# Optimization experiments

Measured on AMD Instinct MI355X. Metric: run time of the kernel, lower is better.

Reference implementation:

```python
import jax, jax.numpy as jnp
import numpy as np

MARGIN = 0.02
EPS = 1e-12


def setup_inputs() -> dict:
    key = jax.random.key(0)
    n, d, k = 4096, 128, 4  # n anchors, embed dim, instances per class
    inputs = jax.random.normal(key, (n, d), dtype=jnp.float32)
    # Balanced, class-grouped batch (required by the original resize trick):
    # label of sample i is i // k.
    targets = (jnp.arange(n) // k).astype(jnp.int32)
    return {"inputs": inputs, "targets": targets, "num_instances": k}


def reference(inputs, targets, num_instances):
    n = inputs.shape[0]
    k = num_instances  # static python int

    # Pairwise euclidean distances (same math as euclidean_dist)
    sq = jnp.sum(inputs * inputs, axis=1, keepdims=True)  # [n,1]
    dist = sq + sq.T - 2.0 * (inputs @ inputs.T)          # [n,n]
    dist = jnp.sqrt(jnp.clip(dist, EPS, None))

    # Structured pos/neg indices for a grouped balanced batch
    # (equivalent to masked_select + resize in the original).
    row = jnp.arange(n)
    class_start = (row // k) * k        # first index of anchor's class block
    pos_in_class = row % k              # anchor's slot within its class
    o_pos = jnp.arange(k - 1)
    # same-class indices excluding self -> [n, k-1]
    pos_idx = class_start[:, None] + o_pos[None, :] + (o_pos[None, :] >= pos_in_class[:, None])
    o_neg = jnp.arange(n - k)
    # all indices outside the anchor's class block -> [n, n-k]
    neg_idx = o_neg[None, :] + k * (o_neg[None, :] >= class_start[:, None])

    pos_dist = dist[row[:, None], pos_idx]  # [n, k-1]
    neg_dist = dist[row[:, None], neg_idx]  # [n, n-k]

    # Triplet margin matrix per anchor: trip[i, m, j] = d_pos[i,j] - d_neg[i,m] + margin
    trip = pos_dist[:, None, :] - neg_dist[:, :, None] + MARGIN  # [n, n-k, k-1]
    mask = trip > 0
    num_valid = jnp.sum(mask)
    total = jnp.sum(jnp.where(mask, trip, 0.0))
    denom = jnp.maximum(num_valid, 1).astype(trip.dtype)
    loss = jnp.where(num_valid > 0, total / denom, jnp.zeros((), trip.dtype))

    per_anchor_valid = jnp.sum(mask, axis=(1, 2))  # [n]
    accuracy = jnp.mean((per_anchor_valid == 0).astype(jnp.float32))
    pos_d = jnp.mean(pos_dist)
    neg_d = jnp.mean(neg_dist)
    return loss, accuracy, pos_d, neg_d
```

## Files before the change

### kernel.cpp

```cpp
#include <hip/hip_runtime.h>

#define NROWS 4096
#define DIM   128
#define KCLS  4
#define NBLK  1056
#define MARGIN_F 0.02f
#define EPS_F    1e-12f

typedef unsigned short ushort_t;
typedef unsigned int   uint_t;
typedef __attribute__((ext_vector_type(8)))  short bf16x8;
typedef __attribute__((ext_vector_type(16))) float f32x16;

__device__ __forceinline__ ushort_t rne_bf16(float v, float& back) {
    uint_t u = __float_as_uint(v);
    uint_t r = (u + 0x7fffu + ((u >> 16) & 1u)) >> 16;
    back = __uint_as_float(r << 16);
    return (ushort_t)r;
}

__device__ __forceinline__ bf16x8 pack8(const ushort_t* h) {
    bf16x8 v;
#pragma unroll
    for (int e = 0; e < 8; ++e) v[e] = (short)h[e];
    return v;
}

__device__ __forceinline__ float fsqrt(float x) {
    float r;
    asm("v_sqrt_f32 %0, %1" : "=v"(r) : "v"(x));
    return r;
}

__device__ __forceinline__ void blk_decode(int bid, int& ti, int& tJ) {
    tJ = (int)((sqrtf((float)(4 * bid + 1)) - 1.0f) * 0.5f);
    while ((tJ + 1) * (tJ + 2) <= bid) ++tJ;
    while (tJ * (tJ + 1) > bid) --tJ;
    ti = bid - tJ * (tJ + 1);
}

__global__ __launch_bounds__(256) void k_prep(
    const float* __restrict__ x,
    float4* __restrict__ spd,
    ushort_t* __restrict__ xf,
    uint_t* __restrict__ imask, uint_t* __restrict__ jmask,
    float* __restrict__ posp)
{
    if (blockIdx.x == 0) {
        const int tt = threadIdx.x;
        if (tt < 128) imask[tt] = 0u; else jmask[tt - 128] = 0u;
    }
    const int wave = threadIdx.x >> 6, lane = threadIdx.x & 63;
    const int cls  = (blockIdx.x << 2) + wave;
    const int r0   = lane >> 4;
    const int cseg = lane & 15;
    const int row  = (cls << 2) + r0;

    const float4* rp = (const float4*)(x + (size_t)row * DIM + (cseg << 3));
    const float4 v0 = rp[0], v1 = rp[1];
    float vs[8] = {v0.x, v0.y, v0.z, v0.w, v1.x, v1.y, v1.z, v1.w};

    float sq = 0.f;
#pragma unroll
    for (int e = 0; e < 8; ++e) sq = fmaf(vs[e], vs[e], sq);
#pragma unroll
    for (int off = 1; off < 16; off <<= 1) sq += __shfl_xor(sq, off, 16);

    float sq4[4];
#pragma unroll
    for (int s = 0; s < 4; ++s) sq4[s] = __shfl(sq, (s << 4) | cseg);

    float dl[3];
#pragma unroll
    for (int delta = 1; delta <= 3; ++delta) {
        const int p = r0 ^ delta;
        float dot = 0.f;
#pragma unroll
        for (int e = 0; e < 8; ++e) {
            const float o = __shfl(vs[e], (p << 4) | cseg);
            dot = fmaf(vs[e], o, dot);
        }
#pragma unroll
        for (int off = 1; off < 16; off <<= 1) dot += __shfl_xor(dot, off, 16);
        dl[delta - 1] = fsqrt(fmaxf(sq4[r0] + sq4[p] - 2.f * dot, EPS_F));
    }
    float po[3];
#pragma unroll
    for (int o = 0; o < 3; ++o) {
        const int s = o + (o >= r0 ? 1 : 0);
        const int d = r0 ^ s;
        po[o] = (d == 1) ? dl[0] : (d == 2) ? dl[1] : dl[2];
    }
    if (cseg == 0) spd[row] = make_float4(sq4[r0], po[0], po[1], po[2]);

    float ppart = (cseg == 0) ? (po[0] + po[1] + po[2]) : 0.f;
#pragma unroll
    for (int off = 32; off; off >>= 1) ppart += __shfl_down(ppart, off);
    __shared__ float pblk[4];
    if (lane == 0) pblk[wave] = ppart;
    __syncthreads();
    if (threadIdx.x == 0)
        posp[blockIdx.x] = pblk[0] + pblk[1] + pblk[2] + pblk[3];

    ushort_t hs[8], ls[8];
#pragma unroll
    for (int e = 0; e < 8; ++e) {
        float back, d_;
        hs[e] = rne_bf16(vs[e], back);
        ls[e] = rne_bf16(vs[e] - back, d_);
    }
    const int band = row >> 5, L = row & 31, cb = cseg >> 1, sf = cseg & 1;
    ushort_t* dst = xf + ((size_t)((band << 3) + cb) << 1) * 512
                       + (((sf << 5) + L) << 3);
    *(bf16x8*)dst         = pack8(hs);
    *(bf16x8*)(dst + 512) = pack8(ls);
}

__global__ __launch_bounds__(256, 4) void k_tiles(
    const ushort_t* __restrict__ xf,
    const float4* __restrict__ spd,
    uint_t* __restrict__ imask, uint_t* __restrict__ jmask,
    float4* __restrict__ partial)
{
    const int lbid = ((blockIdx.x & 7) * 132) + ((int)blockIdx.x >> 3);
    int ti, tJ;
    blk_decode(lbid, ti, tJ);

    const int t = threadIdx.x, wave = t >> 6, lane = t & 63;
    const int wr = wave >> 1, wc = wave & 1;
    const int col = lane & 31, hi = lane >> 5;
    const int ibase = ti << 6;
    const int tj64 = (tJ << 1) + wc;
    const bool active   = (tj64 >= ti);
    const bool anchor_j = (tj64 > ti);
    const int jb  = (tJ << 2) + (wc << 1);
    const int jg0 = (jb << 5) + col;
    const int jg1 = jg0 + 32;

    __shared__ float4 spd_i[64];
    __shared__ float4 wpart[4];

    float4 myspd;
    if (t < 64) myspd = spd[ibase + t];
    const float4 sj0 = spd[jg0];
    const float4 sj1 = spd[jg1];

    const ushort_t* pa  = xf + (size_t)((ti << 1) + wr) * 8192 + lane * 8;
    const ushort_t* pb0 = xf + (size_t)jb * 8192 + lane * 8;
    const ushort_t* pb1 = pb0 + 8192;

    f32x16 acc0, acc1;
#pragma unroll
    for (int r = 0; r < 16; ++r) { acc0[r] = 0.f; acc1[r] = 0.f; }

#pragma unroll
    for (int c = 0; c < 8; ++c) {
        const bf16x8 ah  = *(const bf16x8*)(pa  + c * 1024);
        const bf16x8 al  = *(const bf16x8*)(pa  + c * 1024 + 512);
        const bf16x8 b0h = *(const bf16x8*)(pb0 + c * 1024);
        const bf16x8 b0l = *(const bf16x8*)(pb0 + c * 1024 + 512);
        const bf16x8 b1h = *(const bf16x8*)(pb1 + c * 1024);
        const bf16x8 b1l = *(const bf16x8*)(pb1 + c * 1024 + 512);
        acc0 = __builtin_amdgcn_mfma_f32_32x32x16_bf16(ah, b0h, acc0, 0, 0, 0);
        acc1 = __builtin_amdgcn_mfma_f32_32x32x16_bf16(ah, b1h, acc1, 0, 0, 0);
        acc0 = __builtin_amdgcn_mfma_f32_32x32x16_bf16(ah, b0l, acc0, 0, 0, 0);
        acc1 = __builtin_amdgcn_mfma_f32_32x32x16_bf16(ah, b1l, acc1, 0, 0, 0);
        acc0 = __builtin_amdgcn_mfma_f32_32x32x16_bf16(al, b0h, acc0, 0, 0, 0);
        acc1 = __builtin_amdgcn_mfma_f32_32x32x16_bf16(al, b1h, acc1, 0, 0, 0);
    }

    if (t < 64) spd_i[t] = myspd;
    __syncthreads();

    float ts = 0.f, ns = 0.f, cntf = 0.f;
    uint_t iam = 0, jany0 = 0, jany1 = 0;

    if (active) {
        const int jcls0 = jg0 >> 2, jcls1 = jg1 >> 2;
        const float nsw = anchor_j ? 2.f : 1.f;
#pragma unroll
        for (int r = 0; r < 16; ++r) {
            const int src = (r & 3) + ((r >> 2) << 3) + (hi << 2);
            const float4 si = spd_i[(wr << 5) + src];
            const int icls = (ibase + (wr << 5) + src) >> 2;
            {
                const float dd = fsqrt(fmaxf(si.x + sj0.x - 2.f * acc0[r], EPS_F));
                const bool skip = !anchor_j && (icls == jcls0);
                if (!skip) {
                    ns += nsw * dd;
                    uint_t v = 0; float h;
                    h = si.y + MARGIN_F - dd; if (h > 0.f) { ts += h; cntf += 1.f; v = 1u; }
                    h = si.z + MARGIN_F - dd; if (h > 0.f) { ts += h; cntf += 1.f; v = 1u; }
                    h = si.w + MARGIN_F - dd; if (h > 0.f) { ts += h; cntf += 1.f; v = 1u; }
                    iam |= v << r;
                    if (anchor_j) {
                        h = sj0.y + MARGIN_F - dd; if (h > 0.f) { ts += h; cntf += 1.f; jany0 = 1u; }
                        h = sj0.z + MARGIN_F - dd; if (h > 0.f) { ts += h; cntf += 1.f; jany0 = 1u; }
                        h = sj0.w + MARGIN_F - dd; if (h > 0.f) { ts += h; cntf += 1.f; jany0 = 1u; }
                    }
                }
            }
            {
                const float dd = fsqrt(fmaxf(si.x + sj1.x - 2.f * acc1[r], EPS_F));
                const bool skip = !anchor_j && (icls == jcls1);
                if (!skip) {
                    ns += nsw * dd;
                    uint_t v = 0; float h;
                    h = si.y + MARGIN_F - dd; if (h > 0.f) { ts += h; cntf += 1.f; v = 1u; }
                    h = si.z + MARGIN_F - dd; if (h > 0.f) { ts += h; cntf += 1.f; v = 1u; }
                    h = si.w + MARGIN_F - dd; if (h > 0.f) { ts += h; cntf += 1.f; v = 1u; }
                    iam |= v << r;
                    if (anchor_j) {
                        h = sj1.y + MARGIN_F - dd; if (h > 0.f) { ts += h; cntf += 1.f; jany1 = 1u; }
                        h = sj1.z + MARGIN_F - dd; if (h > 0.f) { ts += h; cntf += 1.f; jany1 = 1u; }
                        h = sj1.w + MARGIN_F - dd; if (h > 0.f) { ts += h; cntf += 1.f; jany1 = 1u; }
                    }
                }
            }
        }

        uint_t iam_all = iam;
#pragma unroll
        for (int off = 1; off < 32; off <<= 1)
            iam_all |= __shfl_xor(iam_all, off);
        uint_t rowmask = 0;
#pragma unroll
        for (int r = 0; r < 16; ++r)
            if ((iam_all >> r) & 1u)
                rowmask |= 1u << ((r & 3) + ((r >> 2) << 3) + (hi << 2));
        if ((lane == 0 || lane == 32) && rowmask)
            atomicOr(&imask[(ti << 1) + wr], rowmask);

        if (anchor_j) {
            const unsigned long long b0 = __ballot(jany0 != 0);
            const uint_t m0 = (uint_t)b0 | (uint_t)(b0 >> 32);
            if (lane == 0 && m0) atomicOr(&jmask[jb], m0);
            const unsigned long long b1 = __ballot(jany1 != 0);
            const uint_t m1 = (uint_t)b1 | (uint_t)(b1 >> 32);
            if (lane == 0 && m1) atomicOr(&jmask[jb + 1], m1);
        }
    }

#pragma unroll
    for (int off = 32; off; off >>= 1) {
        ts   += __shfl_down(ts, off);
        ns   += __shfl_down(ns, off);
        cntf += __shfl_down(cntf, off);
    }
    if (lane == 0) wpart[wave] = make_float4(ts, ns, cntf, 0.f);
    __syncthreads();
    if (t == 0) {
        float4 s = wpart[0];
        s.x += wpart[1].x + wpart[2].x + wpart[3].x;
        s.y += wpart[1].y + wpart[2].y + wpart[3].y;
        s.z += wpart[1].z + wpart[2].z + wpart[3].z;
        partial[lbid] = s;
    }
}

__global__ void k_final(const uint_t* __restrict__ imask,
                        const uint_t* __restrict__ jmask,
                        const float4* __restrict__ partial,
                        const float* __restrict__ posp,
                        float* __restrict__ out)
{
    const int t = threadIdx.x;
    const int lane = t & 63, wave = t >> 6;
    double ts = 0.0, ns = 0.0, cnt = 0.0, ps = 0.0;
    uint_t zc = 0;

    for (int idx = t; idx < NBLK; idx += 256) {
        const float4 p = partial[idx];
        ts += (double)p.x; ns += (double)p.y; cnt += (double)p.z;
    }
    ps = (double)posp[t];
    if (t < 128) zc = 32u - (uint_t)__popc(imask[t] | jmask[t]);

#pragma unroll
    for (int off = 32; off; off >>= 1) {
        ts  += __shfl_down(ts, off);
        ns  += __shfl_down(ns, off);
        cnt += __shfl_down(cnt, off);
        ps  += __shfl_down(ps, off);
        zc  += __shfl_down(zc, off);
    }
    __shared__ double s0[4], s1[4], s2[4], s3[4];
    __shared__ uint_t s4[4];
    if (lane == 0) { s0[wave]=ts; s1[wave]=ns; s2[wave]=cnt; s3[wave]=ps; s4[wave]=zc; }
    __syncthreads();
    if (t == 0) {
        double a0=0, a1=0, a2=0, a3=0; uint_t a4=0;
#pragma unroll
        for (int w = 0; w < 4; ++w) { a0+=s0[w]; a1+=s1[w]; a2+=s2[w]; a3+=s3[w]; a4+=s4[w]; }
        out[0] = (float)(a2 > 0.0 ? a0 / a2 : 0.0);
        out[1] = (float)((double)a4 / (double)NROWS);
        out[2] = (float)(a3 / ((double)NROWS * 3.0));
        out[3] = (float)(a1 / ((double)NROWS * (double)(NROWS - KCLS)));
    }
}

extern "C" void kernel_launch(void* const* d_in, const int* in_sizes, int n_in,
                              void* d_out, int out_size, void* d_ws, size_t ws_size,
                              hipStream_t stream)
{
    const float* x = (const float*)d_in[0];
    float* out = (float*)d_out;
    char* ws = (char*)d_ws;

    uint_t*   imask   = (uint_t*)(ws + 0);
    uint_t*   jmask   = (uint_t*)(ws + 512);
    float*    posp    = (float*)(ws + 1024);
    float4*   spd     = (float4*)(ws + 2048);
    float4*   partial = (float4*)(ws + 2048 + 65536);
    ushort_t* xf      = (ushort_t*)(ws + 2048 + 65536 + 16896);

    k_prep<<<256, 256, 0, stream>>>(x, spd, xf, imask, jmask, posp);
    k_tiles<<<NBLK, 256, 0, stream>>>(xf, spd, imask, jmask, partial);
    k_final<<<1, 256, 0, stream>>>(imask, jmask, partial, posp, out);
}
```

Measured before the change: 115.0 us.

## Stage operand fragments in LDS via direct global-to-LDS loads in tile kernel

Each block now loads the six 32-row bands of hi/lo bf16 fragments it needs into shared memory using global_load_lds, then feeds the MFMAs from LDS instead of per-wave global loads. The goal is to stop the two waves that share a band from loading it twice, and to get coalesced bulk transfers. In exchange the block uses about 96 KB of LDS and launch_bounds drops to 3 blocks per CU, which may reduce occupancy. The partial-sum index also changes from lbid to blockIdx.x, which is a harmless permutation because the final kernel only sums the partials.

```diff
diff --git a/kernel.cpp b/kernel.cpp
--- a/kernel.cpp
+++ b/kernel.cpp
@@ -30,6 +30,12 @@
     float r;
     asm("v_sqrt_f32 %0, %1" : "=v"(r) : "v"(x));
     return r;
+}
+
+__device__ __forceinline__ void gload_lds16(const void* g, void* l) {
+    __builtin_amdgcn_global_load_lds(
+        (const __attribute__((address_space(1))) unsigned int*)g,
+        (__attribute__((address_space(3))) unsigned int*)l, 16, 0, 0);
 }
 
 __device__ __forceinline__ void blk_decode(int bid, int& ti, int& tJ) {
@@ -116,7 +122,7 @@
     *(bf16x8*)(dst + 512) = pack8(ls);
 }
 
-__global__ __launch_bounds__(256, 4) void k_tiles(
+__global__ __launch_bounds__(256, 3) void k_tiles(
     const ushort_t* __restrict__ xf,
     const float4* __restrict__ spd,
     uint_t* __restrict__ imask, uint_t* __restrict__ jmask,
@@ -137,6 +143,7 @@
     const int jg0 = (jb << 5) + col;
     const int jg1 = jg0 + 32;
 
+    __shared__ ushort_t frag[12 * 512 * 8];
     __shared__ float4 spd_i[64];
     __shared__ float4 wpart[4];
 
@@ -145,9 +152,28 @@
     const float4 sj0 = spd[jg0];
     const float4 sj1 = spd[jg1];
 
-    const ushort_t* pa  = xf + (size_t)((ti << 1) + wr) * 8192 + lane * 8;
-    const ushort_t* pb0 = xf + (size_t)jb * 8192 + lane * 8;
-    const ushort_t* pb1 = pb0 + 8192;
+    int gband[6];
+    gband[0] = (ti << 1);     gband[1] = (ti << 1) + 1;
+    gband[2] = (tJ << 2);     gband[3] = (tJ << 2) + 1;
+    gband[4] = (tJ << 2) + 2; gband[5] = (tJ << 2) + 3;
+
+#pragma unroll
+    for (int it = 0; it < 24; ++it) {
+        const int ub = it * 256 + (wave << 6);
+        const int u  = ub + lane;
+        const int bp = u >> 9, rem = u & 511;
+        const int s = rem >> 5, row = rem & 31;
+        const size_t goff = (size_t)gband[bp >> 1] * 8192
+                          + ((s >> 1) << 10) + ((bp & 1) << 9)
+                          + ((s & 1) << 8) + (row << 3);
+        gload_lds16(xf + goff, &frag[(size_t)ub << 3]);
+    }
+    if (t < 64) spd_i[t] = myspd;
+    __syncthreads();
+
+    const int bpA = wr << 1;
+    const int bpB0 = 4 + (wc << 2);
+    const int bpB1 = 6 + (wc << 2);
 
     f32x16 acc0, acc1;
 #pragma unroll
@@ -155,12 +181,14 @@
 
 #pragma unroll
     for (int c = 0; c < 8; ++c) {
-        const bf16x8 ah  = *(const bf16x8*)(pa  + c * 1024);
-        const bf16x8 al  = *(const bf16x8*)(pa  + c * 1024 + 512);
-        const bf16x8 b0h = *(const bf16x8*)(pb0 + c * 1024);
-        const bf16x8 b0l = *(const bf16x8*)(pb0 + c * 1024 + 512);
-        const bf16x8 b1h = *(const bf16x8*)(pb1 + c * 1024);
-        const bf16x8 b1l = *(const bf16x8*)(pb1 + c * 1024 + 512);
+        const int s = (c << 1) + hi;
+        const int so = (s << 5) + col;
+        const bf16x8 ah  = *(const bf16x8*)&frag[(((bpA     ) << 9) + so) << 3];
+        const bf16x8 al  = *(const bf16x8*)&frag[(((bpA  + 1) << 9) + so) << 3];
+        const bf16x8 b0h = *(const bf16x8*)&frag[(((bpB0    ) << 9) + so) << 3];
+        const bf16x8 b0l = *(const bf16x8*)&frag[(((bpB0 + 1) << 9) + so) << 3];
+        const bf16x8 b1h = *(const bf16x8*)&frag[(((bpB1    ) << 9) + so) << 3];
+        const bf16x8 b1l = *(const bf16x8*)&frag[(((bpB1 + 1) << 9) + so) << 3];
         acc0 = __builtin_amdgcn_mfma_f32_32x32x16_bf16(ah, b0h, acc0, 0, 0, 0);
         acc1 = __builtin_amdgcn_mfma_f32_32x32x16_bf16(ah, b1h, acc1, 0, 0, 0);
         acc0 = __builtin_amdgcn_mfma_f32_32x32x16_bf16(ah, b0l, acc0, 0, 0, 0);
@@ -168,9 +196,6 @@
         acc0 = __builtin_amdgcn_mfma_f32_32x32x16_bf16(al, b0h, acc0, 0, 0, 0);
         acc1 = __builtin_amdgcn_mfma_f32_32x32x16_bf16(al, b1h, acc1, 0, 0, 0);
     }
-
-    if (t < 64) spd_i[t] = myspd;
-    __syncthreads();
 
     float ts = 0.f, ns = 0.f, cntf = 0.f;
     uint_t iam = 0, jany0 = 0, jany1 = 0;
@@ -254,7 +279,7 @@
         s.x += wpart[1].x + wpart[2].x + wpart[3].x;
         s.y += wpart[1].y + wpart[2].y + wpart[3].y;
         s.z += wpart[1].z + wpart[2].z + wpart[3].z;
-        partial[lbid] = s;
+        partial[blockIdx.x] = s;
     }
 }
 
```

Measured after the change: 113.2 us. No clear change (-1.6%).

## Issue all operand loads before MFMAs and drop XCD block remapping

Applied to the files above, without the earlier changes.

Replaces the unrolled load-then-MFMA loop with explicit registers so all 48 vector loads for the 8 K-chunks are issued up front, then all MFMAs run. This exposes maximum memory-level parallelism per wave. Launch bounds are relaxed from 4 to 1 blocks per CU so the compiler can use the extra VGPRs. The XCD-aware block index swizzle is also removed. The risks are lower occupancy and worse L2 locality across XCDs.

```diff
diff --git a/kernel.cpp b/kernel.cpp
--- a/kernel.cpp
+++ b/kernel.cpp
@@ -116,15 +116,29 @@
     *(bf16x8*)(dst + 512) = pack8(ls);
 }
 
-__global__ __launch_bounds__(256, 4) void k_tiles(
+#define LDF(dst, base, off) dst = *(const bf16x8*)((base) + (off))
+
+#define LDB(S, c) \
+    LDF(aH##S, pa, (c) * 1024);  LDF(aL##S, pa, (c) * 1024 + 512); \
+    LDF(bH##S, pb0, (c) * 1024); LDF(bL##S, pb0, (c) * 1024 + 512); \
+    LDF(cH##S, pb1, (c) * 1024); LDF(cL##S, pb1, (c) * 1024 + 512);
+
+#define MM(S) \
+    acc0 = __builtin_amdgcn_mfma_f32_32x32x16_bf16(aH##S, bH##S, acc0, 0, 0, 0); \
+    acc1 = __builtin_amdgcn_mfma_f32_32x32x16_bf16(aH##S, cH##S, acc1, 0, 0, 0); \
+    acc0 = __builtin_amdgcn_mfma_f32_32x32x16_bf16(aH##S, bL##S, acc0, 0, 0, 0); \
+    acc1 = __builtin_amdgcn_mfma_f32_32x32x16_bf16(aH##S, cL##S, acc1, 0, 0, 0); \
+    acc0 = __builtin_amdgcn_mfma_f32_32x32x16_bf16(aL##S, bH##S, acc0, 0, 0, 0); \
+    acc1 = __builtin_amdgcn_mfma_f32_32x32x16_bf16(aL##S, cH##S, acc1, 0, 0, 0);
+
+__global__ __launch_bounds__(256, 1) void k_tiles(
     const ushort_t* __restrict__ xf,
     const float4* __restrict__ spd,
     uint_t* __restrict__ imask, uint_t* __restrict__ jmask,
     float4* __restrict__ partial)
 {
-    const int lbid = ((blockIdx.x & 7) * 132) + ((int)blockIdx.x >> 3);
     int ti, tJ;
-    blk_decode(lbid, ti, tJ);
+    blk_decode((int)blockIdx.x, ti, tJ);
 
     const int t = threadIdx.x, wave = t >> 6, lane = t & 63;
     const int wr = wave >> 1, wc = wave & 1;
@@ -153,21 +167,18 @@
 #pragma unroll
     for (int r = 0; r < 16; ++r) { acc0[r] = 0.f; acc1[r] = 0.f; }
 
-#pragma unroll
-    for (int c = 0; c < 8; ++c) {
-        const bf16x8 ah  = *(const bf16x8*)(pa  + c * 1024);
-        const bf16x8 al  = *(const bf16x8*)(pa  + c * 1024 + 512);
-        const bf16x8 b0h = *(const bf16x8*)(pb0 + c * 1024);
-        const bf16x8 b0l = *(const bf16x8*)(pb0 + c * 1024 + 512);
-        const bf16x8 b1h = *(const bf16x8*)(pb1 + c * 1024);
-        const bf16x8 b1l = *(const bf16x8*)(pb1 + c * 1024 + 512);
-        acc0 = __builtin_amdgcn_mfma_f32_32x32x16_bf16(ah, b0h, acc0, 0, 0, 0);
-        acc1 = __builtin_amdgcn_mfma_f32_32x32x16_bf16(ah, b1h, acc1, 0, 0, 0);
-        acc0 = __builtin_amdgcn_mfma_f32_32x32x16_bf16(ah, b0l, acc0, 0, 0, 0);
-        acc1 = __builtin_amdgcn_mfma_f32_32x32x16_bf16(ah, b1l, acc1, 0, 0, 0);
-        acc0 = __builtin_amdgcn_mfma_f32_32x32x16_bf16(al, b0h, acc0, 0, 0, 0);
-        acc1 = __builtin_amdgcn_mfma_f32_32x32x16_bf16(al, b1h, acc1, 0, 0, 0);
-    }
+    bf16x8 aH0, aL0, bH0, bL0, cH0, cL0;
+    bf16x8 aH1, aL1, bH1, bL1, cH1, cL1;
+    bf16x8 aH2, aL2, bH2, bL2, cH2, cL2;
+    bf16x8 aH3, aL3, bH3, bL3, cH3, cL3;
+    bf16x8 aH4, aL4, bH4, bL4, cH4, cL4;
+    bf16x8 aH5, aL5, bH5, bL5, cH5, cL5;
+    bf16x8 aH6, aL6, bH6, bL6, cH6, cL6;
+    bf16x8 aH7, aL7, bH7, bL7, cH7, cL7;
+
+    LDB(0, 0) LDB(1, 1) LDB(2, 2) LDB(3, 3)
+    LDB(4, 4) LDB(5, 5) LDB(6, 6) LDB(7, 7)
+    MM(0) MM(1) MM(2) MM(3) MM(4) MM(5) MM(6) MM(7)
 
     if (t < 64) spd_i[t] = myspd;
     __syncthreads();
@@ -254,7 +265,7 @@
         s.x += wpart[1].x + wpart[2].x + wpart[3].x;
         s.y += wpart[1].y + wpart[2].y + wpart[3].y;
         s.z += wpart[1].z + wpart[2].z + wpart[3].z;
-        partial[lbid] = s;
+        partial[blockIdx.x] = s;
     }
 }
 
```

Result: faster. 110.5 us (-3.9%).
